# Kernel tuning notes

Hardware: AMD Instinct MI355X
Metric: run time of the kernel (lower is better)

The kernel has to match this reference:

```python
import jax, jax.numpy as jnp
import numpy as np

D_MODEL = 1024
NUM_HEADS = 16
DEPTH = D_MODEL // NUM_HEADS  # 64
B, S = 4, 2048
NEG_BIG = -1000000000.0


def setup_inputs() -> dict:
    key = jax.random.key(0)
    ks = jax.random.split(key, 9)
    # Glorot-uniform per-head projection weights, stacked over heads: [H, d_model, depth]
    lim_qkv = np.sqrt(6.0 / (D_MODEL + DEPTH)).astype(np.float32)
    lim_o = np.sqrt(6.0 / (D_MODEL + D_MODEL)).astype(np.float32)
    x = jax.random.normal(ks[0], (B, S, D_MODEL), dtype=jnp.float32)
    attention_mask = jnp.ones((B, S, 1), dtype=jnp.float32)
    Wq = jax.random.uniform(ks[1], (NUM_HEADS, D_MODEL, DEPTH), jnp.float32, -lim_qkv, lim_qkv)
    Wk = jax.random.uniform(ks[2], (NUM_HEADS, D_MODEL, DEPTH), jnp.float32, -lim_qkv, lim_qkv)
    Wv = jax.random.uniform(ks[3], (NUM_HEADS, D_MODEL, DEPTH), jnp.float32, -lim_qkv, lim_qkv)
    bq = jnp.zeros((NUM_HEADS, DEPTH), jnp.float32)
    bk = jnp.zeros((NUM_HEADS, DEPTH), jnp.float32)
    bv = jnp.zeros((NUM_HEADS, DEPTH), jnp.float32)
    Wo = jax.random.uniform(ks[4], (D_MODEL, D_MODEL), jnp.float32, -lim_o, lim_o)
    bo = jnp.zeros((D_MODEL,), jnp.float32)
    return {"x": x, "attention_mask": attention_mask, "Wq": Wq, "bq": bq,
            "Wk": Wk, "bk": bk, "Wv": Wv, "bv": bv, "Wo": Wo, "bo": bo}


def reference(x, attention_mask, Wq, bq, Wk, bk, Wv, bv, Wo, bo):
    # Batched over heads (same math as the per-head Python loop + concat).
    # x: [B,S,D]; Wq/Wk/Wv: [H,D,depth]; bq/bk/bv: [H,depth]
    q = jnp.einsum('bsd,hde->bhse', x, Wq) + bq[None, :, None, :]
    k = jnp.einsum('bsd,hde->bhse', x, Wk) + bk[None, :, None, :]
    v = jnp.einsum('bsd,hde->bhse', x, Wv) + bv[None, :, None, :]
    scale = 1.0 / jnp.sqrt(jnp.asarray(DEPTH, dtype=x.dtype))
    scores = jnp.einsum('bhse,bhte->bhst', q, k) * scale  # [B,H,S,S]
    # original: mask.transpose(-2,-1) -> [B,1,S], broadcast over query rows; add head axis
    mask_t = jnp.swapaxes(attention_mask, -2, -1)[:, None]  # [B,1,1,S]
    scores = scores + (1.0 - mask_t) * NEG_BIG
    probs = jax.nn.softmax(scores, axis=-1)
    z = jnp.einsum('bhst,bhte->bhse', probs, v)  # [B,H,S,depth]
    # concat heads along feature dim (head order matches torch.cat order)
    multi_head = jnp.transpose(z, (0, 2, 1, 3)).reshape(x.shape[0], x.shape[1], NUM_HEADS * DEPTH)
    return multi_head @ Wo + bo
```

## Files before the change

kernel.cpp:

```cpp
#include <hip/hip_runtime.h>

#define NH 16
#define DEP 64
#define DM 1024
#define BB 4
#define SS 2048

typedef __attribute__((ext_vector_type(8))) __bf16 bf16x8;
typedef __attribute__((ext_vector_type(4))) __bf16 bf16x4;
typedef __attribute__((ext_vector_type(2))) __bf16 bf16x2;
typedef __attribute__((ext_vector_type(4))) float f32x4;
typedef __attribute__((ext_vector_type(4))) unsigned u32x4;
typedef __attribute__((ext_vector_type(2))) unsigned u32x2;
typedef unsigned short u16;

#define MFMA_BF16(A, B, C) __builtin_amdgcn_mfma_f32_16x16x32_bf16(A, B, C, 0, 0, 0)

#define SCL 0.18033688011112042f
#define LOG2E 1.4426950408889634f

__device__ __forceinline__ u16 f2bf(float f) {
  unsigned u = __builtin_bit_cast(unsigned, f);
  u += 0x7fffu + ((u >> 16) & 1u);
  return (u16)(u >> 16);
}

__device__ __forceinline__ unsigned pk2(float a, float b) {
  bf16x2 t;
  t[0] = (__bf16)a; t[1] = (__bf16)b;
  return __builtin_bit_cast(unsigned, t);
}

__device__ __forceinline__ void gload_lds16(const u16* g, u16* l) {
  __builtin_amdgcn_global_load_lds((const __attribute__((address_space(1))) void*)g,
                                   (__attribute__((address_space(3))) void*)l, 16, 0, 0);
}

__global__ __launch_bounds__(256) void k_cvt_x(const float* __restrict__ x, u16* __restrict__ xb) {
  int i = (blockIdx.x * 256 + threadIdx.x) * 4;
  float4 v = *(const float4*)(x + i);
  ushort4 o;
  o.x = f2bf(v.x); o.y = f2bf(v.y); o.z = f2bf(v.z); o.w = f2bf(v.w);
  *(ushort4*)(xb + i) = o;
}

__global__ __launch_bounds__(256) void k_pack_qkv(const float* __restrict__ Wq, const float* __restrict__ Wk,
                                                  const float* __restrict__ Wv,
                                                  const float* __restrict__ bq, const float* __restrict__ bk,
                                                  const float* __restrict__ bv,
                                                  u16* __restrict__ wt, float* __restrict__ biasN) {
  __shared__ float lt[64][65];
  int k0 = blockIdx.x * 64;
  int z = blockIdx.y;
  int which = z >> 4, h = z & 15;
  const float* W = which == 0 ? Wq : (which == 1 ? Wk : Wv);
  const float* bsrc = which == 0 ? bq : (which == 1 ? bk : bv);
  const float* src = W + (size_t)h * DM * DEP;
  int t = threadIdx.x;
#pragma unroll
  for (int p = 0; p < 16; ++p) {
    int li = p * 256 + t;
    int r = li >> 6, c = li & 63;
    lt[r][c] = src[(size_t)(k0 + r) * 64 + c];
  }
  __syncthreads();
  int woff = which * DM + h * 64;
#pragma unroll
  for (int p = 0; p < 16; ++p) {
    int li = p * 256 + t;
    int r = li >> 6, c = li & 63;
    wt[(size_t)(woff + r) * DM + k0 + c] = f2bf(lt[c][r]);
  }
  if (blockIdx.x == 0 && t < 64) biasN[woff + t] = bsrc[h * 64 + t];
}

__global__ __launch_bounds__(256) void k_pack_wo(const float* __restrict__ Wo, u16* __restrict__ wot) {
  __shared__ float lt[64][65];
  int k0 = blockIdx.x * 64, n0 = blockIdx.y * 64;
  int t = threadIdx.x;
#pragma unroll
  for (int p = 0; p < 16; ++p) {
    int li = p * 256 + t;
    int r = li >> 6, c = li & 63;
    lt[r][c] = Wo[(size_t)(k0 + r) * DM + n0 + c];
  }
  __syncthreads();
#pragma unroll
  for (int p = 0; p < 16; ++p) {
    int li = p * 256 + t;
    int r = li >> 6, c = li & 63;
    wot[(size_t)(n0 + r) * DM + k0 + c] = f2bf(lt[c][r]);
  }
}

__global__ __launch_bounds__(256) void k_maskbias(const float* __restrict__ mask, float* __restrict__ mb) {
  int i = blockIdx.x * 256 + threadIdx.x;
  mb[i] = (1.0f - mask[i]) * (-1000000000.0f * LOG2E);
}

__global__ __launch_bounds__(256) void k_gemm_qkv(const u16* __restrict__ xb, const u16* __restrict__ wt,
                                                  const float* __restrict__ biasN,
                                                  u16* __restrict__ qb, u16* __restrict__ kb,
                                                  u16* __restrict__ vtb) {
  __shared__ u16 lA[128 * 32];
  __shared__ u16 lB[128 * 32];
  const int tid = threadIdx.x;
  const int lane = tid & 63, w = tid >> 6;
  const int m0 = blockIdx.x * 128, n0 = blockIdx.y * 128;
  const int wm = (w >> 1) * 64, wn = (w & 1) * 64;
  const int fr = lane & 15, fg = lane >> 4;
  const int bidx = tid * 16;
  const int row0 = bidx >> 6, c0 = (bidx & 63) >> 1;
  f32x4 acc[4][4] = {};
  for (int k0 = 0; k0 < DM; k0 += 32) {
    __syncthreads();
    gload_lds16(xb + (size_t)(m0 + row0) * DM + k0 + c0, lA + w * 512);
    gload_lds16(xb + (size_t)(m0 + row0 + 64) * DM + k0 + c0, lA + 2048 + w * 512);
    gload_lds16(wt + (size_t)(n0 + row0) * DM + k0 + c0, lB + w * 512);
    gload_lds16(wt + (size_t)(n0 + row0 + 64) * DM + k0 + c0, lB + 2048 + w * 512);
    __syncthreads();
    bf16x8 af[4], bfr[4];
#pragma unroll
    for (int i = 0; i < 4; ++i) {
      af[i] = *(const bf16x8*)&lA[(wm + i * 16 + fr) * 32 + fg * 8];
      bfr[i] = *(const bf16x8*)&lB[(wn + i * 16 + fr) * 32 + fg * 8];
    }
#pragma unroll
    for (int i = 0; i < 4; ++i)
#pragma unroll
      for (int j = 0; j < 4; ++j)
        acc[i][j] = MFMA_BF16(af[i], bfr[j], acc[i][j]);
  }
#pragma unroll
  for (int i = 0; i < 4; ++i)
#pragma unroll
    for (int j = 0; j < 4; ++j) {
      int n = n0 + wn + j * 16 + fr;
      float bn = biasN[n];
      int which = n >> 10, rem = n & 1023, h = rem >> 6, d = rem & 63;
#pragma unroll
      for (int r = 0; r < 4; ++r) {
        int m = m0 + wm + i * 16 + fg * 4 + r;
        int b = m >> 11, s = m & 2047;
        float val = acc[i][j][r] + bn;
        if (which == 0)      qb[(((size_t)(b * NH + h) * SS + s) << 6) + d] = f2bf(val * SCL);
        else if (which == 1) kb[(((size_t)(b * NH + h) * SS + s) << 6) + d] = f2bf(val);
        else                 vtb[(((size_t)(b * NH + h) * 64 + d) << 11) + s] = f2bf(val);
      }
    }
}

__global__ __launch_bounds__(256, 2) void k_attn(const u16* __restrict__ qb, const u16* __restrict__ kb,
                                                 const u16* __restrict__ vtb, const float* __restrict__ mbias,
                                                 u16* __restrict__ zb) {
  __shared__ u16 sK[2][64 * 64];
  __shared__ u16 sV[2][64 * 64];
  const int bh = blockIdx.y;
  const int b = bh >> 4, h = bh & 15;
  const int tid = threadIdx.x, lane = tid & 63, w = tid >> 6;
  const int q0 = blockIdx.x * 256 + w * 64;
  const u16* Q  = qb  + (size_t)bh * SS * 64;
  const u16* K  = kb  + (size_t)bh * SS * 64;
  const u16* VT = vtb + (size_t)bh * 64 * SS;
  const float* mbb = mbias + b * SS;
  const int fr = lane & 15, fg = lane >> 4;
  const int fr7 = fr & 7;
  const int rsub = lane >> 3;
  const int cg = (lane & 7) ^ rsub;
  const int kc0 = (fg ^ fr7) * 16;
  const int kc1 = ((4 + fg) ^ fr7) * 16;
  const int fg1 = fg >> 1, fgb = (fg & 1) * 8;
  const int cX0 = (((fg1)     ^ fr7)) * 16 + fgb;
  const int cX1 = (((2 + (fg1 ^ 1)) ^ fr7)) * 16 + fgb;
  const int cY0 = (((4 + fg1) ^ fr7)) * 16 + fgb;
  const int cY1 = (((6 + (fg1 ^ 1)) ^ fr7)) * 16 + fgb;
  bf16x8 qlo[4], qhi[4];
#pragma unroll
  for (int qf = 0; qf < 4; ++qf) {
    qlo[qf] = *(const bf16x8*)&Q[(q0 + 16 * qf + fr) * 64 + fg * 8];
    qhi[qf] = *(const bf16x8*)&Q[(q0 + 16 * qf + fr) * 64 + 32 + fg * 8];
  }
  float lrun[4] = {0.f, 0.f, 0.f, 0.f};
  f32x4 o[4][4] = {};

#pragma unroll
  for (int j = 0; j < 2; ++j) {
    int i = w * 2 + j;
    gload_lds16(K + (size_t)(8 * i + rsub) * 64 + cg * 8, &sK[0][i * 512]);
    gload_lds16(VT + (size_t)(8 * i + rsub) * SS + cg * 8, &sV[0][i * 512]);
  }
  __syncthreads();

  for (int t = 0; t < 32; ++t) {
    const int cur = t & 1;
    if (t < 31) {
      const int kvn = (t + 1) * 64;
#pragma unroll
      for (int j = 0; j < 2; ++j) {
        int i = w * 2 + j;
        gload_lds16(K + (size_t)(kvn + 8 * i + rsub) * 64 + cg * 8, &sK[cur ^ 1][i * 512]);
        gload_lds16(VT + (size_t)(8 * i + rsub) * SS + kvn + cg * 8, &sV[cur ^ 1][i * 512]);
      }
    }
    const int kv = t * 64;
    const char* Kb = (const char*)&sK[cur][0];
    const char* Vb = (const char*)&sV[cur][0];
    bf16x8 klo[4], khi[4];
#pragma unroll
    for (int kt = 0; kt < 4; ++kt) {
      klo[kt] = *(const bf16x8*)(Kb + (kt * 16 + fr) * 128 + kc0);
      khi[kt] = *(const bf16x8*)(Kb + (kt * 16 + fr) * 128 + kc1);
    }
    u32x2 vx0[4], vx1[4], vy0[4], vy1[4];
#pragma unroll
    for (int dc = 0; dc < 4; ++dc) {
      const char* rb = Vb + (dc * 16 + fr) * 128;
      vx0[dc] = *(const u32x2*)(rb + cX0);
      vx1[dc] = *(const u32x2*)(rb + cX1);
      vy0[dc] = *(const u32x2*)(rb + cY0);
      vy1[dc] = *(const u32x2*)(rb + cY1);
    }
#pragma unroll
    for (int qf = 0; qf < 4; ++qf) {
      f32x4 sc[4];
      __builtin_amdgcn_s_setprio(1);
#pragma unroll
      for (int kt = 0; kt < 4; ++kt) {
        f32x4 mb4 = *(const f32x4*)(mbb + kv + kt * 16 + fg * 4);
        sc[kt] = MFMA_BF16(khi[kt], qhi[qf], MFMA_BF16(klo[kt], qlo[qf], mb4));
      }
      __builtin_amdgcn_s_setprio(0);
      float e00 = __builtin_amdgcn_exp2f(sc[0][0]), e01 = __builtin_amdgcn_exp2f(sc[0][1]);
      float e02 = __builtin_amdgcn_exp2f(sc[0][2]), e03 = __builtin_amdgcn_exp2f(sc[0][3]);
      float e10 = __builtin_amdgcn_exp2f(sc[1][0]), e11 = __builtin_amdgcn_exp2f(sc[1][1]);
      float e12 = __builtin_amdgcn_exp2f(sc[1][2]), e13 = __builtin_amdgcn_exp2f(sc[1][3]);
      float e20 = __builtin_amdgcn_exp2f(sc[2][0]), e21 = __builtin_amdgcn_exp2f(sc[2][1]);
      float e22 = __builtin_amdgcn_exp2f(sc[2][2]), e23 = __builtin_amdgcn_exp2f(sc[2][3]);
      float e30 = __builtin_amdgcn_exp2f(sc[3][0]), e31 = __builtin_amdgcn_exp2f(sc[3][1]);
      float e32 = __builtin_amdgcn_exp2f(sc[3][2]), e33 = __builtin_amdgcn_exp2f(sc[3][3]);
      lrun[qf] += ((e00 + e01) + (e02 + e03)) + ((e10 + e11) + (e12 + e13))
                + ((e20 + e21) + (e22 + e23)) + ((e30 + e31) + (e32 + e33));
      unsigned w00 = pk2(e00, e01), w01 = pk2(e02, e03);
      unsigned w10 = pk2(e10, e11), w11 = pk2(e12, e13);
      unsigned w20 = pk2(e20, e21), w21 = pk2(e22, e23);
      unsigned w30 = pk2(e30, e31), w31 = pk2(e32, e33);
      unsigned x2 = (unsigned)__shfl_xor((int)w10, 32);
      unsigned x3 = (unsigned)__shfl_xor((int)w11, 32);
      unsigned y2 = (unsigned)__shfl_xor((int)w30, 32);
      unsigned y3 = (unsigned)__shfl_xor((int)w31, 32);
      u32x4 ux = {w00, w01, x2, x3};
      u32x4 uy = {w20, w21, y2, y3};
      bf16x8 paX = __builtin_bit_cast(bf16x8, ux);
      bf16x8 paY = __builtin_bit_cast(bf16x8, uy);
      __builtin_amdgcn_s_setprio(1);
#pragma unroll
      for (int dc = 0; dc < 4; ++dc) {
        u32x4 vxw = {vx0[dc][0], vx0[dc][1], vx1[dc][0], vx1[dc][1]};
        u32x4 vyw = {vy0[dc][0], vy0[dc][1], vy1[dc][0], vy1[dc][1]};
        bf16x8 vX = __builtin_bit_cast(bf16x8, vxw);
        bf16x8 vY = __builtin_bit_cast(bf16x8, vyw);
        o[qf][dc] = MFMA_BF16(paX, vX, o[qf][dc]);
        o[qf][dc] = MFMA_BF16(paY, vY, o[qf][dc]);
      }
      __builtin_amdgcn_s_setprio(0);
    }
    __syncthreads();
  }
#pragma unroll
  for (int qf = 0; qf < 4; ++qf) {
    float l = lrun[qf];
    l += __shfl_xor(l, 16);
    l += __shfl_xor(l, 32);
#pragma unroll
    for (int r = 0; r < 4; ++r) {
      float linv = 1.0f / __shfl(l, 4 * fg + r);
      int s = q0 + 16 * qf + 4 * fg + r;
#pragma unroll
      for (int dc = 0; dc < 4; ++dc)
        zb[(size_t)(b * SS + s) * DM + h * 64 + dc * 16 + fr] = f2bf(o[qf][dc][r] * linv);
    }
  }
}

__global__ __launch_bounds__(256) void k_gemm_out(const u16* __restrict__ zb, const u16* __restrict__ wot,
                                                  const float* __restrict__ bo, float* __restrict__ out) {
  __shared__ u16 lA[128 * 32];
  __shared__ u16 lB[128 * 32];
  const int tid = threadIdx.x;
  const int lane = tid & 63, w = tid >> 6;
  const int m0 = blockIdx.x * 128, n0 = blockIdx.y * 128;
  const int wm = (w >> 1) * 64, wn = (w & 1) * 64;
  const int fr = lane & 15, fg = lane >> 4;
  const int bidx = tid * 16;
  const int row0 = bidx >> 6, c0 = (bidx & 63) >> 1;
  f32x4 acc[4][4] = {};
  for (int k0 = 0; k0 < DM; k0 += 32) {
    __syncthreads();
    gload_lds16(zb + (size_t)(m0 + row0) * DM + k0 + c0, lA + w * 512);
    gload_lds16(zb + (size_t)(m0 + row0 + 64) * DM + k0 + c0, lA + 2048 + w * 512);
    gload_lds16(wot + (size_t)(n0 + row0) * DM + k0 + c0, lB + w * 512);
    gload_lds16(wot + (size_t)(n0 + row0 + 64) * DM + k0 + c0, lB + 2048 + w * 512);
    __syncthreads();
    bf16x8 af[4], bfr[4];
#pragma unroll
    for (int i = 0; i < 4; ++i) {
      af[i] = *(const bf16x8*)&lA[(wm + i * 16 + fr) * 32 + fg * 8];
      bfr[i] = *(const bf16x8*)&lB[(wn + i * 16 + fr) * 32 + fg * 8];
    }
#pragma unroll
    for (int i = 0; i < 4; ++i)
#pragma unroll
      for (int j = 0; j < 4; ++j)
        acc[i][j] = MFMA_BF16(af[i], bfr[j], acc[i][j]);
  }
#pragma unroll
  for (int i = 0; i < 4; ++i)
#pragma unroll
    for (int j = 0; j < 4; ++j) {
      int n = n0 + wn + j * 16 + fr;
      float bn = bo[n];
#pragma unroll
      for (int r = 0; r < 4; ++r) {
        int m = m0 + wm + i * 16 + fg * 4 + r;
        out[(size_t)m * DM + n] = acc[i][j][r] + bn;
      }
    }
}

extern "C" void kernel_launch(void* const* d_in, const int* in_sizes, int n_in,
                              void* d_out, int out_size, void* d_ws, size_t ws_size,
                              hipStream_t stream) {
  const float* x    = (const float*)d_in[0];
  const float* mask = (const float*)d_in[1];
  const float* Wq   = (const float*)d_in[2];
  const float* bq   = (const float*)d_in[3];
  const float* Wk   = (const float*)d_in[4];
  const float* bk   = (const float*)d_in[5];
  const float* Wv   = (const float*)d_in[6];
  const float* bv   = (const float*)d_in[7];
  const float* Wo   = (const float*)d_in[8];
  const float* bo   = (const float*)d_in[9];
  char* ws = (char*)d_ws;
  u16*   xb    = (u16*)(ws + 0);
  u16*   zb    = xb;
  u16*   wt    = (u16*)(ws + 16777216);
  u16*   wot   = (u16*)(ws + 23068672);
  float* biasN = (float*)(ws + 25165824);
  float* mb    = (float*)(ws + 25178112);
  u16*   qb    = (u16*)(ws + 25210880);
  u16*   kb    = (u16*)(ws + 41988096);
  u16*   vtb   = (u16*)(ws + 58765312);
  float* out   = (float*)d_out;

  k_cvt_x<<<dim3(8192), dim3(256), 0, stream>>>(x, xb);
  k_pack_qkv<<<dim3(16, 48), dim3(256), 0, stream>>>(Wq, Wk, Wv, bq, bk, bv, wt, biasN);
  k_pack_wo<<<dim3(16, 16), dim3(256), 0, stream>>>(Wo, wot);
  k_maskbias<<<dim3(32), dim3(256), 0, stream>>>(mask, mb);
  k_gemm_qkv<<<dim3(64, 24), dim3(256), 0, stream>>>(xb, wt, biasN, qb, kb, vtb);
  k_attn<<<dim3(8, 64), dim3(256), 0, stream>>>(qb, kb, vtb, mb, zb);
  k_gemm_out<<<dim3(64, 8), dim3(256), 0, stream>>>(zb, wot, bo, out);
}
```

Measured before the change: 219.7 us.

## Stage 128-key KV tiles per barrier in attention kernel to halve syncs

The attention kernel now loads 128 keys of K and V^T into double-buffered LDS per stage and processes them as two 64-key sub-tiles, so the loop runs 16 iterations instead of 32. This halves the number of __syncthreads barriers and gives each async load more compute to hide behind. The V^T tile changes to 128-wide rows with a new XOR swizzle, and the mask bias loads are hoisted out of the per-query-fragment loop. LDS use doubles to 64KB per block, which may limit occupancy at 2 blocks per CU.

After: 423.7 us. 1.93x slower.

```diff
diff --git a/kernel.cpp b/kernel.cpp
--- a/kernel.cpp
+++ b/kernel.cpp
@@ -153,8 +153,8 @@
 __global__ __launch_bounds__(256, 2) void k_attn(const u16* __restrict__ qb, const u16* __restrict__ kb,
                                                  const u16* __restrict__ vtb, const float* __restrict__ mbias,
                                                  u16* __restrict__ zb) {
-  __shared__ u16 sK[2][64 * 64];
-  __shared__ u16 sV[2][64 * 64];
+  __shared__ u16 sK[2][128 * 64];
+  __shared__ u16 sV[2][64 * 128];
   const int bh = blockIdx.y;
   const int b = bh >> 4, h = bh & 15;
   const int tid = threadIdx.x, lane = tid & 63, w = tid >> 6;
@@ -166,14 +166,15 @@
   const int fr = lane & 15, fg = lane >> 4;
   const int fr7 = fr & 7;
   const int rsub = lane >> 3;
-  const int cg = (lane & 7) ^ rsub;
+  const int kcg = (lane & 7) ^ rsub;
+  const int vds = lane >> 4;
   const int kc0 = (fg ^ fr7) * 16;
   const int kc1 = ((4 + fg) ^ fr7) * 16;
   const int fg1 = fg >> 1, fgb = (fg & 1) * 8;
-  const int cX0 = (((fg1)     ^ fr7)) * 16 + fgb;
-  const int cX1 = (((2 + (fg1 ^ 1)) ^ fr7)) * 16 + fgb;
-  const int cY0 = (((4 + fg1) ^ fr7)) * 16 + fgb;
-  const int cY1 = (((6 + (fg1 ^ 1)) ^ fr7)) * 16 + fgb;
+  const int cX0 = ((fg1)           ^ fr7) * 16 + fgb;
+  const int cX1 = ((2 + (fg1 ^ 1)) ^ fr7) * 16 + fgb;
+  const int cY0 = ((4 + fg1)       ^ fr7) * 16 + fgb;
+  const int cY1 = ((6 + (fg1 ^ 1)) ^ fr7) * 16 + fgb;
   bf16x8 qlo[4], qhi[4];
 #pragma unroll
   for (int qf = 0; qf < 4; ++qf) {
@@ -183,86 +184,89 @@
   float lrun[4] = {0.f, 0.f, 0.f, 0.f};
   f32x4 o[4][4] = {};
 
-#pragma unroll
-  for (int j = 0; j < 2; ++j) {
-    int i = w * 2 + j;
-    gload_lds16(K + (size_t)(8 * i + rsub) * 64 + cg * 8, &sK[0][i * 512]);
-    gload_lds16(VT + (size_t)(8 * i + rsub) * SS + cg * 8, &sV[0][i * 512]);
-  }
+  auto stage = [&](int t, int buf) {
+    const int kvn = t * 128;
+#pragma unroll
+    for (int j = 0; j < 4; ++j) {
+      int i = w * 4 + j;
+      gload_lds16(K + (size_t)(kvn + 8 * i + rsub) * 64 + kcg * 8, &sK[buf][i * 512]);
+      int d = 4 * i + vds;
+      int vcg = (lane & 15) ^ (d & 7);
+      gload_lds16(VT + (size_t)d * SS + kvn + vcg * 8, &sV[buf][i * 512]);
+    }
+  };
+
+  stage(0, 0);
   __syncthreads();
 
-  for (int t = 0; t < 32; ++t) {
+  for (int t = 0; t < 16; ++t) {
     const int cur = t & 1;
-    if (t < 31) {
-      const int kvn = (t + 1) * 64;
-#pragma unroll
-      for (int j = 0; j < 2; ++j) {
-        int i = w * 2 + j;
-        gload_lds16(K + (size_t)(kvn + 8 * i + rsub) * 64 + cg * 8, &sK[cur ^ 1][i * 512]);
-        gload_lds16(VT + (size_t)(8 * i + rsub) * SS + kvn + cg * 8, &sV[cur ^ 1][i * 512]);
-      }
-    }
-    const int kv = t * 64;
-    const char* Kb = (const char*)&sK[cur][0];
-    const char* Vb = (const char*)&sV[cur][0];
-    bf16x8 klo[4], khi[4];
-#pragma unroll
-    for (int kt = 0; kt < 4; ++kt) {
-      klo[kt] = *(const bf16x8*)(Kb + (kt * 16 + fr) * 128 + kc0);
-      khi[kt] = *(const bf16x8*)(Kb + (kt * 16 + fr) * 128 + kc1);
-    }
-    u32x2 vx0[4], vx1[4], vy0[4], vy1[4];
-#pragma unroll
-    for (int dc = 0; dc < 4; ++dc) {
-      const char* rb = Vb + (dc * 16 + fr) * 128;
-      vx0[dc] = *(const u32x2*)(rb + cX0);
-      vx1[dc] = *(const u32x2*)(rb + cX1);
-      vy0[dc] = *(const u32x2*)(rb + cY0);
-      vy1[dc] = *(const u32x2*)(rb + cY1);
-    }
-#pragma unroll
-    for (int qf = 0; qf < 4; ++qf) {
-      f32x4 sc[4];
-      __builtin_amdgcn_s_setprio(1);
+    if (t < 15) stage(t + 1, cur ^ 1);
+#pragma unroll
+    for (int s = 0; s < 2; ++s) {
+      const int kv = t * 128 + s * 64;
+      const char* Kb = (const char*)&sK[cur][0] + s * 8192;
+      const char* Vb = (const char*)&sV[cur][0] + s * 128;
+      f32x4 mbv[4];
+#pragma unroll
+      for (int kt = 0; kt < 4; ++kt) mbv[kt] = *(const f32x4*)(mbb + kv + kt * 16 + fg * 4);
+      bf16x8 klo[4], khi[4];
 #pragma unroll
       for (int kt = 0; kt < 4; ++kt) {
-        f32x4 mb4 = *(const f32x4*)(mbb + kv + kt * 16 + fg * 4);
-        sc[kt] = MFMA_BF16(khi[kt], qhi[qf], MFMA_BF16(klo[kt], qlo[qf], mb4));
-      }
-      __builtin_amdgcn_s_setprio(0);
-      float e00 = __builtin_amdgcn_exp2f(sc[0][0]), e01 = __builtin_amdgcn_exp2f(sc[0][1]);
-      float e02 = __builtin_amdgcn_exp2f(sc[0][2]), e03 = __builtin_amdgcn_exp2f(sc[0][3]);
-      float e10 = __builtin_amdgcn_exp2f(sc[1][0]), e11 = __builtin_amdgcn_exp2f(sc[1][1]);
-      float e12 = __builtin_amdgcn_exp2f(sc[1][2]), e13 = __builtin_amdgcn_exp2f(sc[1][3]);
-      float e20 = __builtin_amdgcn_exp2f(sc[2][0]), e21 = __builtin_amdgcn_exp2f(sc[2][1]);
-      float e22 = __builtin_amdgcn_exp2f(sc[2][2]), e23 = __builtin_amdgcn_exp2f(sc[2][3]);
-      float e30 = __builtin_amdgcn_exp2f(sc[3][0]), e31 = __builtin_amdgcn_exp2f(sc[3][1]);
-      float e32 = __builtin_amdgcn_exp2f(sc[3][2]), e33 = __builtin_amdgcn_exp2f(sc[3][3]);
-      lrun[qf] += ((e00 + e01) + (e02 + e03)) + ((e10 + e11) + (e12 + e13))
-                + ((e20 + e21) + (e22 + e23)) + ((e30 + e31) + (e32 + e33));
-      unsigned w00 = pk2(e00, e01), w01 = pk2(e02, e03);
-      unsigned w10 = pk2(e10, e11), w11 = pk2(e12, e13);
-      unsigned w20 = pk2(e20, e21), w21 = pk2(e22, e23);
-      unsigned w30 = pk2(e30, e31), w31 = pk2(e32, e33);
-      unsigned x2 = (unsigned)__shfl_xor((int)w10, 32);
-      unsigned x3 = (unsigned)__shfl_xor((int)w11, 32);
-      unsigned y2 = (unsigned)__shfl_xor((int)w30, 32);
-      unsigned y3 = (unsigned)__shfl_xor((int)w31, 32);
-      u32x4 ux = {w00, w01, x2, x3};
-      u32x4 uy = {w20, w21, y2, y3};
-      bf16x8 paX = __builtin_bit_cast(bf16x8, ux);
-      bf16x8 paY = __builtin_bit_cast(bf16x8, uy);
-      __builtin_amdgcn_s_setprio(1);
+        klo[kt] = *(const bf16x8*)(Kb + (kt * 16 + fr) * 128 + kc0);
+        khi[kt] = *(const bf16x8*)(Kb + (kt * 16 + fr) * 128 + kc1);
+      }
+      u32x2 vx0[4], vx1[4], vy0[4], vy1[4];
 #pragma unroll
       for (int dc = 0; dc < 4; ++dc) {
-        u32x4 vxw = {vx0[dc][0], vx0[dc][1], vx1[dc][0], vx1[dc][1]};
-        u32x4 vyw = {vy0[dc][0], vy0[dc][1], vy1[dc][0], vy1[dc][1]};
-        bf16x8 vX = __builtin_bit_cast(bf16x8, vxw);
-        bf16x8 vY = __builtin_bit_cast(bf16x8, vyw);
-        o[qf][dc] = MFMA_BF16(paX, vX, o[qf][dc]);
-        o[qf][dc] = MFMA_BF16(paY, vY, o[qf][dc]);
-      }
-      __builtin_amdgcn_s_setprio(0);
+        const char* rb = Vb + (dc * 16 + fr) * 256;
+        vx0[dc] = *(const u32x2*)(rb + cX0);
+        vx1[dc] = *(const u32x2*)(rb + cX1);
+        vy0[dc] = *(const u32x2*)(rb + cY0);
+        vy1[dc] = *(const u32x2*)(rb + cY1);
+      }
+#pragma unroll
+      for (int qf = 0; qf < 4; ++qf) {
+        f32x4 sc[4];
+        __builtin_amdgcn_s_setprio(1);
+#pragma unroll
+        for (int kt = 0; kt < 4; ++kt)
+          sc[kt] = MFMA_BF16(khi[kt], qhi[qf], MFMA_BF16(klo[kt], qlo[qf], mbv[kt]));
+        __builtin_amdgcn_s_setprio(0);
+        float e00 = __builtin_amdgcn_exp2f(sc[0][0]), e01 = __builtin_amdgcn_exp2f(sc[0][1]);
+        float e02 = __builtin_amdgcn_exp2f(sc[0][2]), e03 = __builtin_amdgcn_exp2f(sc[0][3]);
+        float e10 = __builtin_amdgcn_exp2f(sc[1][0]), e11 = __builtin_amdgcn_exp2f(sc[1][1]);
+        float e12 = __builtin_amdgcn_exp2f(sc[1][2]), e13 = __builtin_amdgcn_exp2f(sc[1][3]);
+        float e20 = __builtin_amdgcn_exp2f(sc[2][0]), e21 = __builtin_amdgcn_exp2f(sc[2][1]);
+        float e22 = __builtin_amdgcn_exp2f(sc[2][2]), e23 = __builtin_amdgcn_exp2f(sc[2][3]);
+        float e30 = __builtin_amdgcn_exp2f(sc[3][0]), e31 = __builtin_amdgcn_exp2f(sc[3][1]);
+        float e32 = __builtin_amdgcn_exp2f(sc[3][2]), e33 = __builtin_amdgcn_exp2f(sc[3][3]);
+        lrun[qf] += ((e00 + e01) + (e02 + e03)) + ((e10 + e11) + (e12 + e13))
+                  + ((e20 + e21) + (e22 + e23)) + ((e30 + e31) + (e32 + e33));
+        unsigned w00 = pk2(e00, e01), w01 = pk2(e02, e03);
+        unsigned w10 = pk2(e10, e11), w11 = pk2(e12, e13);
+        unsigned w20 = pk2(e20, e21), w21 = pk2(e22, e23);
+        unsigned w30 = pk2(e30, e31), w31 = pk2(e32, e33);
+        unsigned x2 = (unsigned)__shfl_xor((int)w10, 32);
+        unsigned x3 = (unsigned)__shfl_xor((int)w11, 32);
+        unsigned y2 = (unsigned)__shfl_xor((int)w30, 32);
+        unsigned y3 = (unsigned)__shfl_xor((int)w31, 32);
+        u32x4 ux = {w00, w01, x2, x3};
+        u32x4 uy = {w20, w21, y2, y3};
+        bf16x8 paX = __builtin_bit_cast(bf16x8, ux);
+        bf16x8 paY = __builtin_bit_cast(bf16x8, uy);
+        __builtin_amdgcn_s_setprio(1);
+#pragma unroll
+        for (int dc = 0; dc < 4; ++dc) {
+          u32x4 vxw = {vx0[dc][0], vx0[dc][1], vx1[dc][0], vx1[dc][1]};
+          u32x4 vyw = {vy0[dc][0], vy0[dc][1], vy1[dc][0], vy1[dc][1]};
+          bf16x8 vX = __builtin_bit_cast(bf16x8, vxw);
+          bf16x8 vY = __builtin_bit_cast(bf16x8, vyw);
+          o[qf][dc] = MFMA_BF16(paX, vX, o[qf][dc]);
+          o[qf][dc] = MFMA_BF16(paY, vY, o[qf][dc]);
+        }
+        __builtin_amdgcn_s_setprio(0);
+      }
     }
     __syncthreads();
   }
```
